# Optimization experiments

Hardware: AMD Instinct MI355X
Metric: run time of the kernel (lower is better)

The kernel has to match this reference:

```python
import jax, jax.numpy as jnp
import numpy as np
import math

NUM_HEADS = 16
HEAD_DIM = 64
D_MODEL = NUM_HEADS * HEAD_DIM  # 1024
B, S = 4, 2048

def setup_inputs() -> dict:
    key = jax.random.key(0)
    ks = jax.random.split(key, 8)
    sd = 1.0 / math.sqrt(D_MODEL)
    return {
        "hidden_states": jax.random.normal(ks[0], (B, S, D_MODEL), jnp.float32),
        "attention_mask": jnp.zeros((B, 1, 1, S), jnp.float32),
        "Wq": jax.random.normal(ks[1], (D_MODEL, D_MODEL), jnp.float32) * sd,
        "bq": jnp.zeros((D_MODEL,), jnp.float32),
        "Wk": jax.random.normal(ks[2], (D_MODEL, D_MODEL), jnp.float32) * sd,
        "bk": jnp.zeros((D_MODEL,), jnp.float32),
        "Wv": jax.random.normal(ks[3], (D_MODEL, D_MODEL), jnp.float32) * sd,
        "bv": jnp.zeros((D_MODEL,), jnp.float32),
    }

def _split_heads(x):
    # [B, S, D] -> [B, H, S, hd]
    b, s, _ = x.shape
    return x.reshape(b, s, NUM_HEADS, HEAD_DIM).transpose(0, 2, 1, 3)

def reference(hidden_states, attention_mask, Wq, bq, Wk, bk, Wv, bv):
    # Linear projections (torch nn.Linear: x @ W.T + b)
    q = _split_heads(hidden_states @ Wq.T + bq)
    k = _split_heads(hidden_states @ Wk.T + bk)
    v = _split_heads(hidden_states @ Wv.T + bv)
    scale = 1.0 / math.sqrt(HEAD_DIM)
    # [B, H, Sq, Sk] attention scores, fully materialized as in the original
    scores = jnp.einsum("bhqd,bhkd->bhqk", q, k) * scale + attention_mask
    # relusq replacement for softmax
    probs = jnp.square(jax.nn.relu(scores))
    ctx = jnp.einsum("bhqk,bhkd->bhqd", probs, v)  # [B, H, S, hd]
    b = ctx.shape[0]
    return ctx.transpose(0, 2, 1, 3).reshape(b, -1, D_MODEL)
```

## Files before the change

### kernel.cpp

```cpp
#include <hip/hip_runtime.h>


typedef __bf16 bf16x8 __attribute__((ext_vector_type(8)));
typedef __bf16 bf16x4 __attribute__((ext_vector_type(4)));
typedef __bf16 bf16x2 __attribute__((ext_vector_type(2)));
typedef short  s16x4  __attribute__((ext_vector_type(4)));
typedef float  f32x4  __attribute__((ext_vector_type(4)));
typedef float  f32x16 __attribute__((ext_vector_type(16)));
typedef float  floatx4 __attribute__((ext_vector_type(4)));
typedef unsigned u32x2 __attribute__((ext_vector_type(2)));
typedef unsigned u32x4 __attribute__((ext_vector_type(4)));

#define MFMA16(a, b, c) __builtin_amdgcn_mfma_f32_16x16x32_bf16(a, b, c, 0, 0, 0)
#define MFMA32(a, b, c) __builtin_amdgcn_mfma_f32_32x32x16_bf16(a, b, c, 0, 0, 0)

#define WAITCNT_VM0() __builtin_amdgcn_s_waitcnt(0x0F70)
#define WAITCNT_VM6() __builtin_amdgcn_s_waitcnt(0x0F76)
#define BARRIER() __builtin_amdgcn_s_barrier()
#define SETPRIO(p) __builtin_amdgcn_s_setprio(p)

__device__ __forceinline__ void glds16(const __bf16* g, __bf16* l) {
    __builtin_amdgcn_global_load_lds(
        (const __attribute__((address_space(1))) void*)g,
        (__attribute__((address_space(3))) void*)l, 16, 0, 0);
}

__global__ __launch_bounds__(256) void convert_kernel(
    const float* __restrict__ X, const float* __restrict__ Wq,
    const float* __restrict__ Wk, const float* __restrict__ Wv,
    __bf16* __restrict__ Xb, __bf16* __restrict__ Wqb,
    __bf16* __restrict__ Wkb, __bf16* __restrict__ Wvb)
{
    int blk = blockIdx.x;
    const float* src; __bf16* dst; size_t base;
    if (blk < 4096)      { src = X;  dst = Xb;  base = (size_t)blk * 2048; }
    else if (blk < 4608) { src = Wq; dst = Wqb; base = (size_t)(blk - 4096) * 2048; }
    else if (blk < 5120) { src = Wk; dst = Wkb; base = (size_t)(blk - 4608) * 2048; }
    else                 { src = Wv; dst = Wvb; base = (size_t)(blk - 5120) * 2048; }
    size_t off = base + (size_t)threadIdx.x * 8;
    floatx4 a = *(const floatx4*)(src + off);
    floatx4 c = *(const floatx4*)(src + off + 4);
    bf16x8 o;
    o[0] = (__bf16)a[0]; o[1] = (__bf16)a[1]; o[2] = (__bf16)a[2]; o[3] = (__bf16)a[3];
    o[4] = (__bf16)c[0]; o[5] = (__bf16)c[1]; o[6] = (__bf16)c[2]; o[7] = (__bf16)c[3];
    *(bf16x8*)(dst + off) = o;
}

__global__ __launch_bounds__(512, 2) void qkv_gemm_kernel(
    const __bf16* __restrict__ Xb,
    const __bf16* __restrict__ Wqb, const __bf16* __restrict__ Wkb,
    const __bf16* __restrict__ Wvb,
    const float* __restrict__ bq, const float* __restrict__ bk,
    const float* __restrict__ bv,
    __bf16* __restrict__ qws, __bf16* __restrict__ kws, __bf16* __restrict__ vws)
{
    __shared__ __bf16 As[3][256 * 64];
    __shared__ __bf16 Bs[3][128 * 64];

    const int tid  = threadIdx.x;
    const int lane = tid & 63;
    const int wave = tid >> 6;
    const int quad = lane >> 4;
    const int l16  = lane & 15;
    const int m0   = blockIdx.y * 256;

    const int sel = blockIdx.x >> 3;
    const bool vmode = (sel == 2);
    const __bf16* Wb = (sel == 0) ? Wqb : (sel == 1) ? Wkb : Wvb;
    const float* bias = (sel == 0) ? bq : (sel == 1) ? bk : bv;
    __bf16* outp = (sel == 0) ? qws : (sel == 1) ? kws : vws;
    const int n0 = (blockIdx.x & 7) * 128;

    const int wA = vmode ? (wave & 3) * 64 : (wave >> 2) * 64;
    const int wB = vmode ? (wave >> 2) * 64 : (wave & 3) * 64;

    const int srow = lane >> 3;
    const int schk = lane & 7;

    f32x4 acc[4][4] = {};

#define QKV_STAGE_A(bb, kt, i) { \
        int rb_ = wave * 32 + (i) * 8; int r_ = rb_ + srow; \
        int c_ = schk ^ (r_ & 7); \
        glds16(Xb + (size_t)(m0 + r_) * 1024 + (kt) * 64 + c_ * 8, \
               &As[bb][rb_ * 64]); }
#define QKV_STAGE_B(bb, kt, i) { \
        int rb_ = wave * 16 + (i) * 8; int r_ = rb_ + srow; \
        int c_ = schk ^ (r_ & 7); \
        glds16(Wb + (size_t)(n0 + r_) * 1024 + (kt) * 64 + c_ * 8, \
               &Bs[bb][rb_ * 64]); }

    #pragma unroll
    for (int i = 0; i < 4; ++i) QKV_STAGE_A(0, 0, i);
    #pragma unroll
    for (int i = 0; i < 2; ++i) QKV_STAGE_B(0, 0, i);
    #pragma unroll
    for (int i = 0; i < 4; ++i) QKV_STAGE_A(1, 1, i);
    #pragma unroll
    for (int i = 0; i < 2; ++i) QKV_STAGE_B(1, 1, i);
    WAITCNT_VM6();
    BARRIER();

    for (int s = 0; s < 16; ++s) {
        const int cb  = s % 3;
        const int pb  = (s + 2) % 3;
        const int kt2 = (s + 2) & 15;
        const __bf16* Pa_ = vmode ? &As[cb][0] : &Bs[cb][0];
        const __bf16* Pb_ = vmode ? &Bs[cb][0] : &As[cb][0];

        #pragma unroll
        for (int p = 0; p < 2; ++p) {
            bf16x8 af[4], bfr[4];
            #pragma unroll
            for (int a = 0; a < 4; ++a)
                af[a] = *(const bf16x8*)&Pa_[(wA + a * 16 + l16) * 64 +
                                             (((p * 4 + quad) ^ (l16 & 7)) * 8)];
            #pragma unroll
            for (int bb = 0; bb < 4; ++bb)
                bfr[bb] = *(const bf16x8*)&Pb_[(wB + bb * 16 + l16) * 64 +
                                               (((p * 4 + quad) ^ (l16 & 7)) * 8)];
            QKV_STAGE_A(pb, kt2, 2 * p);
            QKV_STAGE_A(pb, kt2, 2 * p + 1);
            QKV_STAGE_B(pb, kt2, p);

            if (p == 1) WAITCNT_VM6();
            BARRIER();

            SETPRIO(1);
            #pragma unroll
            for (int a = 0; a < 4; ++a)
                #pragma unroll
                for (int bb = 0; bb < 4; ++bb)
                    acc[a][bb] = MFMA16(af[a], bfr[bb], acc[a][bb]);
            SETPRIO(0);
            BARRIER();
        }
    }

#undef QKV_STAGE_A
#undef QKV_STAGE_B

    if (!vmode) {
        #pragma unroll
        for (int a = 0; a < 4; ++a) {
            int n = n0 + wA + a * 16 + quad * 4;
            floatx4 bv4 = *(const floatx4*)&bias[n];
            int h = n >> 6, d0 = n & 63;
            #pragma unroll
            for (int bb = 0; bb < 4; ++bb) {
                int m = m0 + wB + bb * 16 + l16;
                int bt = m >> 11, ss = m & 2047;
                bf16x4 o;
                #pragma unroll
                for (int r = 0; r < 4; ++r)
                    o[r] = (__bf16)(acc[a][bb][r] + bv4[r]);
                *(bf16x4*)&outp[((size_t)(bt * 16 + h) * 2048 + ss) * 64 + d0] = o;
            }
        }
    } else {
        #pragma unroll
        for (int a = 0; a < 4; ++a) {
            int m = m0 + wA + a * 16 + quad * 4;
            int bt = m >> 11, s0 = m & 2047;
            #pragma unroll
            for (int bb = 0; bb < 4; ++bb) {
                int n = n0 + wB + bb * 16 + l16;
                float bvv = bias[n];
                int h = n >> 6, d = n & 63;
                bf16x4 o;
                #pragma unroll
                for (int r = 0; r < 4; ++r)
                    o[r] = (__bf16)(acc[a][bb][r] + bvv);
                *(bf16x4*)&outp[((size_t)(bt * 16 + h) * 64 + d) * 2048 + s0] = o;
            }
        }
    }
}

__global__ __launch_bounds__(256, 2) void attn_kernel(
    const __bf16* __restrict__ Q, const __bf16* __restrict__ K,
    const __bf16* __restrict__ Vt, const float* __restrict__ mask,
    float* __restrict__ out)
{
    __shared__ __bf16 Ks[2][2][64 * 64];
    __shared__ __bf16 Vs[2][2][64 * 64];
    __shared__ float  Ms[2048];

    const int tid  = threadIdx.x;
    const int lane = tid & 63;
    const int wave = tid >> 6;
    const int l32  = lane & 31;
    const int hi   = lane >> 5;
    const int bh   = blockIdx.x;
    const int b    = bh >> 4;
    const int h    = bh & 15;
    const int q0w  = blockIdx.y * 256 + wave * 64;

    const __bf16* Qb = Q  + (size_t)bh * 2048 * 64;
    const __bf16* Kb = K  + (size_t)bh * 2048 * 64;
    const __bf16* Vb = Vt + (size_t)bh * 64 * 2048;
    const float*  mb = mask + b * 2048;

    const int rb = wave * 16;
    const int sr = rb + (lane >> 3);
    const int sc = ((lane & 7) ^ (sr & 7)) * 8;

    bf16x8 aq[2][4];
    #pragma unroll
    for (int qg = 0; qg < 2; ++qg)
        #pragma unroll
        for (int dk = 0; dk < 4; ++dk)
            aq[qg][dk] = *(const bf16x8*)(Qb +
                (size_t)(q0w + qg * 32 + l32) * 64 + dk * 16 + hi * 8);

    f32x16 co[2][2] = {};

    glds16(Kb + (size_t)sr * 64 + sc,              &Ks[0][0][rb * 64]);
    glds16(Kb + (size_t)(sr + 8) * 64 + sc,        &Ks[0][0][(rb + 8) * 64]);
    glds16(Kb + (size_t)(64 + sr) * 64 + sc,       &Ks[0][1][rb * 64]);
    glds16(Kb + (size_t)(64 + sr + 8) * 64 + sc,   &Ks[0][1][(rb + 8) * 64]);
    glds16(Vb + (size_t)sr * 2048 + sc,            &Vs[0][0][rb * 64]);
    glds16(Vb + (size_t)(sr + 8) * 2048 + sc,      &Vs[0][0][(rb + 8) * 64]);
    glds16(Vb + (size_t)sr * 2048 + 64 + sc,       &Vs[0][1][rb * 64]);
    glds16(Vb + (size_t)(sr + 8) * 2048 + 64 + sc, &Vs[0][1][(rb + 8) * 64]);
    glds16((const __bf16*)mb + (size_t)(wave * 2) * 512 + lane * 8,
           (__bf16*)Ms + (wave * 2) * 512);
    glds16((const __bf16*)mb + (size_t)(wave * 2 + 1) * 512 + lane * 8,
           (__bf16*)Ms + (wave * 2 + 1) * 512);
    WAITCNT_VM0();
    BARRIER();

    for (int t = 0; t < 16; ++t) {
        const int kn = ((t + 1) & 15) * 128;
        const int nb = (t + 1) & 1;
        const int cb = t & 1;
        glds16(Kb + (size_t)(kn + sr) * 64 + sc,            &Ks[nb][0][rb * 64]);
        glds16(Kb + (size_t)(kn + sr + 8) * 64 + sc,        &Ks[nb][0][(rb + 8) * 64]);
        glds16(Kb + (size_t)(kn + 64 + sr) * 64 + sc,       &Ks[nb][1][rb * 64]);
        glds16(Kb + (size_t)(kn + 64 + sr + 8) * 64 + sc,   &Ks[nb][1][(rb + 8) * 64]);
        glds16(Vb + (size_t)sr * 2048 + kn + sc,            &Vs[nb][0][rb * 64]);
        glds16(Vb + (size_t)(sr + 8) * 2048 + kn + sc,      &Vs[nb][0][(rb + 8) * 64]);
        glds16(Vb + (size_t)sr * 2048 + kn + 64 + sc,       &Vs[nb][1][rb * 64]);
        glds16(Vb + (size_t)(sr + 8) * 2048 + kn + 64 + sc, &Vs[nb][1][(rb + 8) * 64]);

        #pragma unroll
        for (int hf = 0; hf < 2; ++hf) {
            const __bf16* Kt = &Ks[cb][hf][0];
            const __bf16* Vtl = &Vs[cb][hf][0];
            const int k0 = t * 128 + hf * 64;

            bf16x8 akf[2][4];
            #pragma unroll
            for (int dk = 0; dk < 4; ++dk) {
                const int c0 = ((dk * 2 + hi) ^ (l32 & 7)) * 8;
                akf[0][dk] = *(const bf16x8*)&Kt[l32 * 64 + c0];
                akf[1][dk] = *(const bf16x8*)&Kt[(32 + l32) * 64 + c0];
            }
            f32x16 st[2][2] = {};
            SETPRIO(1);
            #pragma unroll
            for (int dk = 0; dk < 4; ++dk)
                #pragma unroll
                for (int qg = 0; qg < 2; ++qg) {
                    st[qg][0] = MFMA32(akf[0][dk], aq[qg][dk], st[qg][0]);
                    st[qg][1] = MFMA32(akf[1][dk], aq[qg][dk], st[qg][1]);
                }
            SETPRIO(0);

            bf16x8 paf0[2][2], paf1[2][2];
            const f32x4 zero4 = {};
            #pragma unroll
            for (int qg = 0; qg < 2; ++qg)
                #pragma unroll
                for (int kg = 0; kg < 2; ++kg) {
                    unsigned W[4][2];
                    #pragma unroll
                    for (int G = 0; G < 4; ++G) {
                        f32x4 v;
                        v[0] = st[qg][kg][G * 4 + 0];
                        v[1] = st[qg][kg][G * 4 + 1];
                        v[2] = st[qg][kg][G * 4 + 2];
                        v[3] = st[qg][kg][G * 4 + 3];
                        f32x4 mk = *(const f32x4*)&Ms[k0 + kg * 32 + G * 8 + hi * 4];
                        v = v * 0.125f + mk;
                        v = __builtin_elementwise_max(v, zero4);
                        v = v * v;
                        bf16x2 w0, w1;
                        w0[0] = (__bf16)v[0]; w0[1] = (__bf16)v[1];
                        w1[0] = (__bf16)v[2]; w1[1] = (__bf16)v[3];
                        W[G][0] = __builtin_bit_cast(unsigned, w0);
                        W[G][1] = __builtin_bit_cast(unsigned, w1);
                    }
                    u32x2 s00 = __builtin_amdgcn_permlane32_swap(W[0][0], W[1][0], false, false);
                    u32x2 s01 = __builtin_amdgcn_permlane32_swap(W[0][1], W[1][1], false, false);
                    u32x2 s10 = __builtin_amdgcn_permlane32_swap(W[2][0], W[3][0], false, false);
                    u32x2 s11 = __builtin_amdgcn_permlane32_swap(W[2][1], W[3][1], false, false);
                    u32x4 f0, f1;
                    f0[0] = s00[0]; f0[1] = s01[0]; f0[2] = s00[1]; f0[3] = s01[1];
                    f1[0] = s10[0]; f1[1] = s11[0]; f1[2] = s10[1]; f1[3] = s11[1];
                    paf0[qg][kg] = __builtin_bit_cast(bf16x8, f0);
                    paf1[qg][kg] = __builtin_bit_cast(bf16x8, f1);
                }

            SETPRIO(1);
            #pragma unroll
            for (int kg = 0; kg < 2; ++kg) {
                bf16x8 vb0[2], vb1[2];
                #pragma unroll
                for (int dt = 0; dt < 2; ++dt) {
                    const int d = dt * 32 + l32;
                    const int ch0 = (kg * 4 + hi) ^ (d & 7);
                    const int ch1 = (kg * 4 + 2 + hi) ^ (d & 7);
                    vb0[dt] = *(const bf16x8*)&Vtl[d * 64 + ch0 * 8];
                    vb1[dt] = *(const bf16x8*)&Vtl[d * 64 + ch1 * 8];
                }
                #pragma unroll
                for (int qg = 0; qg < 2; ++qg)
                    #pragma unroll
                    for (int dt = 0; dt < 2; ++dt) {
                        co[qg][dt] = MFMA32(paf0[qg][kg], vb0[dt], co[qg][dt]);
                        co[qg][dt] = MFMA32(paf1[qg][kg], vb1[dt], co[qg][dt]);
                    }
            }
            SETPRIO(0);
        }

        WAITCNT_VM0();
        BARRIER();
    }

    #pragma unroll
    for (int qg = 0; qg < 2; ++qg)
        #pragma unroll
        for (int r = 0; r < 16; ++r) {
            int q = q0w + qg * 32 + (r & 3) + 8 * (r >> 2) + 4 * hi;
            float* orow = &out[(((size_t)b * 2048 + q) * 16 + h) * 64];
            orow[l32]      = co[qg][0][r];
            orow[32 + l32] = co[qg][1][r];
        }
}

extern "C" void kernel_launch(void* const* d_in, const int* in_sizes, int n_in,
                              void* d_out, int out_size, void* d_ws, size_t ws_size,
                              hipStream_t stream) {
    const float* hidden = (const float*)d_in[0];
    const float* mask   = (const float*)d_in[1];
    const float* Wq     = (const float*)d_in[2];
    const float* bq     = (const float*)d_in[3];
    const float* Wk     = (const float*)d_in[4];
    const float* bk     = (const float*)d_in[5];
    const float* Wv     = (const float*)d_in[6];
    const float* bv     = (const float*)d_in[7];
    float* out = (float*)d_out;

    __bf16* qws = (__bf16*)d_ws;
    __bf16* kws = qws + (size_t)64 * 2048 * 64;
    __bf16* vws = kws + (size_t)64 * 2048 * 64;
    __bf16* Xb  = vws + (size_t)64 * 2048 * 64;
    __bf16* Wqb = Xb  + (size_t)8192 * 1024;
    __bf16* Wkb = Wqb + (size_t)1024 * 1024;
    __bf16* Wvb = Wkb + (size_t)1024 * 1024;

    convert_kernel<<<dim3(5632), dim3(256), 0, stream>>>(hidden, Wq, Wk, Wv,
                                                         Xb, Wqb, Wkb, Wvb);
    qkv_gemm_kernel<<<dim3(24, 32), dim3(512), 0, stream>>>(Xb, Wqb, Wkb, Wvb,
                                                            bq, bk, bv,
                                                            qws, kws, vws);
    attn_kernel<<<dim3(64, 8), dim3(256), 0, stream>>>(qws, kws, vws, mask, out);
}
```

Measured before the change: 234.3 us.

## Fuse fp32-to-bf16 conversion into QKV GEMM via register-staged loads

Removes the separate conversion kernel and has the QKV GEMM load fp32 X and W directly into registers, convert them to bf16 and write them to LDS with a two-stage register prefetch pipeline. This drops a full read/write pass over the activations and weights plus one kernel launch. In exchange it gives up async global-to-LDS loads and the three-stage buffer, and it shrinks the tile to 128x128 with 256 threads. Each block now re-reads fp32 data, which doubles global bytes per tile and adds per-block conversion work.

Result: slower. 266.9 us (+13.9%).

```diff
diff --git a/kernel.cpp b/kernel.cpp
--- a/kernel.cpp
+++ b/kernel.cpp
@@ -15,7 +15,6 @@
 #define MFMA32(a, b, c) __builtin_amdgcn_mfma_f32_32x32x16_bf16(a, b, c, 0, 0, 0)
 
 #define WAITCNT_VM0() __builtin_amdgcn_s_waitcnt(0x0F70)
-#define WAITCNT_VM6() __builtin_amdgcn_s_waitcnt(0x0F76)
 #define BARRIER() __builtin_amdgcn_s_barrier()
 #define SETPRIO(p) __builtin_amdgcn_s_setprio(p)
 
@@ -25,130 +24,130 @@
         (__attribute__((address_space(3))) void*)l, 16, 0, 0);
 }
 
-__global__ __launch_bounds__(256) void convert_kernel(
-    const float* __restrict__ X, const float* __restrict__ Wq,
-    const float* __restrict__ Wk, const float* __restrict__ Wv,
-    __bf16* __restrict__ Xb, __bf16* __restrict__ Wqb,
-    __bf16* __restrict__ Wkb, __bf16* __restrict__ Wvb)
-{
-    int blk = blockIdx.x;
-    const float* src; __bf16* dst; size_t base;
-    if (blk < 4096)      { src = X;  dst = Xb;  base = (size_t)blk * 2048; }
-    else if (blk < 4608) { src = Wq; dst = Wqb; base = (size_t)(blk - 4096) * 2048; }
-    else if (blk < 5120) { src = Wk; dst = Wkb; base = (size_t)(blk - 4608) * 2048; }
-    else                 { src = Wv; dst = Wvb; base = (size_t)(blk - 5120) * 2048; }
-    size_t off = base + (size_t)threadIdx.x * 8;
-    floatx4 a = *(const floatx4*)(src + off);
-    floatx4 c = *(const floatx4*)(src + off + 4);
-    bf16x8 o;
-    o[0] = (__bf16)a[0]; o[1] = (__bf16)a[1]; o[2] = (__bf16)a[2]; o[3] = (__bf16)a[3];
-    o[4] = (__bf16)c[0]; o[5] = (__bf16)c[1]; o[6] = (__bf16)c[2]; o[7] = (__bf16)c[3];
-    *(bf16x8*)(dst + off) = o;
-}
-
-__global__ __launch_bounds__(512, 2) void qkv_gemm_kernel(
-    const __bf16* __restrict__ Xb,
-    const __bf16* __restrict__ Wqb, const __bf16* __restrict__ Wkb,
-    const __bf16* __restrict__ Wvb,
+__global__ __launch_bounds__(256) void qkv_gemm_kernel(
+    const float* __restrict__ Xf,
+    const float* __restrict__ Wqf, const float* __restrict__ Wkf,
+    const float* __restrict__ Wvf,
     const float* __restrict__ bq, const float* __restrict__ bk,
     const float* __restrict__ bv,
     __bf16* __restrict__ qws, __bf16* __restrict__ kws, __bf16* __restrict__ vws)
 {
-    __shared__ __bf16 As[3][256 * 64];
-    __shared__ __bf16 Bs[3][128 * 64];
+    __shared__ __bf16 As[2][128 * 64];
+    __shared__ __bf16 Bs[2][128 * 64];
 
     const int tid  = threadIdx.x;
     const int lane = tid & 63;
     const int wave = tid >> 6;
+    const int wm   = (wave >> 1) * 64;
+    const int wn   = (wave & 1) * 64;
     const int quad = lane >> 4;
     const int l16  = lane & 15;
-    const int m0   = blockIdx.y * 256;
+    const int m0   = blockIdx.y * 128;
 
     const int sel = blockIdx.x >> 3;
     const bool vmode = (sel == 2);
-    const __bf16* Wb = (sel == 0) ? Wqb : (sel == 1) ? Wkb : Wvb;
+    const float* Wf = (sel == 0) ? Wqf : (sel == 1) ? Wkf : Wvf;
     const float* bias = (sel == 0) ? bq : (sel == 1) ? bk : bv;
     __bf16* outp = (sel == 0) ? qws : (sel == 1) ? kws : vws;
     const int n0 = (blockIdx.x & 7) * 128;
 
-    const int wA = vmode ? (wave & 3) * 64 : (wave >> 2) * 64;
-    const int wB = vmode ? (wave >> 2) * 64 : (wave & 3) * 64;
+    const int woffA = vmode ? wm : wn;
+    const int woffB = vmode ? wn : wm;
 
     const int srow = lane >> 3;
     const int schk = lane & 7;
 
     f32x4 acc[4][4] = {};
 
-#define QKV_STAGE_A(bb, kt, i) { \
-        int rb_ = wave * 32 + (i) * 8; int r_ = rb_ + srow; \
-        int c_ = schk ^ (r_ & 7); \
-        glds16(Xb + (size_t)(m0 + r_) * 1024 + (kt) * 64 + c_ * 8, \
-               &As[bb][rb_ * 64]); }
-#define QKV_STAGE_B(bb, kt, i) { \
-        int rb_ = wave * 16 + (i) * 8; int r_ = rb_ + srow; \
-        int c_ = schk ^ (r_ & 7); \
-        glds16(Wb + (size_t)(n0 + r_) * 1024 + (kt) * 64 + c_ * 8, \
-               &Bs[bb][rb_ * 64]); }
-
-    #pragma unroll
-    for (int i = 0; i < 4; ++i) QKV_STAGE_A(0, 0, i);
-    #pragma unroll
-    for (int i = 0; i < 2; ++i) QKV_STAGE_B(0, 0, i);
-    #pragma unroll
-    for (int i = 0; i < 4; ++i) QKV_STAGE_A(1, 1, i);
-    #pragma unroll
-    for (int i = 0; i < 2; ++i) QKV_STAGE_B(1, 1, i);
-    WAITCNT_VM6();
-    BARRIER();
+    int rbu[4], ru[4], cu[4];
+    #pragma unroll
+    for (int i = 0; i < 4; ++i) {
+        rbu[i] = wave * 32 + i * 8;
+        ru[i]  = rbu[i] + srow;
+        cu[i]  = (schk ^ (ru[i] & 7)) * 8;
+    }
+
+#define QKV_LOAD(dst, srcp, row, k) { \
+        size_t o_ = (size_t)(row) * 1024 + (size_t)(k); \
+        dst[0] = *(const floatx4*)((srcp) + o_); \
+        dst[1] = *(const floatx4*)((srcp) + o_ + 4); }
+
+#define QKV_CVTW(dstb, rb_, v) { \
+        bf16x8 o_; \
+        o_[0] = (__bf16)v[0][0]; o_[1] = (__bf16)v[0][1]; \
+        o_[2] = (__bf16)v[0][2]; o_[3] = (__bf16)v[0][3]; \
+        o_[4] = (__bf16)v[1][0]; o_[5] = (__bf16)v[1][1]; \
+        o_[6] = (__bf16)v[1][2]; o_[7] = (__bf16)v[1][3]; \
+        *(bf16x8*)&dstb[(rb_) * 64 + lane * 8] = o_; }
+
+    floatx4 ra[4][2], rw[4][2];
+
+    #pragma unroll
+    for (int i = 0; i < 4; ++i) {
+        QKV_LOAD(ra[i], Xf, m0 + ru[i], cu[i]);
+        QKV_LOAD(rw[i], Wf, n0 + ru[i], cu[i]);
+    }
+    #pragma unroll
+    for (int i = 0; i < 4; ++i) {
+        QKV_CVTW(As[0], rbu[i], ra[i]);
+        QKV_CVTW(Bs[0], rbu[i], rw[i]);
+    }
+    __syncthreads();
 
     for (int s = 0; s < 16; ++s) {
-        const int cb  = s % 3;
-        const int pb  = (s + 2) % 3;
-        const int kt2 = (s + 2) & 15;
-        const __bf16* Pa_ = vmode ? &As[cb][0] : &Bs[cb][0];
-        const __bf16* Pb_ = vmode ? &Bs[cb][0] : &As[cb][0];
-
-        #pragma unroll
-        for (int p = 0; p < 2; ++p) {
+        const int kn = ((s + 1) & 15) * 64;
+        const int nb = (s + 1) & 1;
+        const int bc = s & 1;
+
+        #pragma unroll
+        for (int i = 0; i < 4; ++i) {
+            QKV_LOAD(ra[i], Xf, m0 + ru[i], kn + cu[i]);
+            QKV_LOAD(rw[i], Wf, n0 + ru[i], kn + cu[i]);
+        }
+
+        const __bf16* Pa_ = vmode ? &As[bc][0] : &Bs[bc][0];
+        const __bf16* Pb_ = vmode ? &Bs[bc][0] : &As[bc][0];
+
+        SETPRIO(1);
+        #pragma unroll
+        for (int kk8 = 0; kk8 < 8; kk8 += 4) {
             bf16x8 af[4], bfr[4];
             #pragma unroll
             for (int a = 0; a < 4; ++a)
-                af[a] = *(const bf16x8*)&Pa_[(wA + a * 16 + l16) * 64 +
-                                             (((p * 4 + quad) ^ (l16 & 7)) * 8)];
+                af[a] = *(const bf16x8*)&Pa_[(woffA + a * 16 + l16) * 64 +
+                                             (((kk8 + quad) ^ (l16 & 7)) * 8)];
             #pragma unroll
             for (int bb = 0; bb < 4; ++bb)
-                bfr[bb] = *(const bf16x8*)&Pb_[(wB + bb * 16 + l16) * 64 +
-                                               (((p * 4 + quad) ^ (l16 & 7)) * 8)];
-            QKV_STAGE_A(pb, kt2, 2 * p);
-            QKV_STAGE_A(pb, kt2, 2 * p + 1);
-            QKV_STAGE_B(pb, kt2, p);
-
-            if (p == 1) WAITCNT_VM6();
-            BARRIER();
-
-            SETPRIO(1);
+                bfr[bb] = *(const bf16x8*)&Pb_[(woffB + bb * 16 + l16) * 64 +
+                                               (((kk8 + quad) ^ (l16 & 7)) * 8)];
             #pragma unroll
             for (int a = 0; a < 4; ++a)
                 #pragma unroll
                 for (int bb = 0; bb < 4; ++bb)
                     acc[a][bb] = MFMA16(af[a], bfr[bb], acc[a][bb]);
-            SETPRIO(0);
-            BARRIER();
-        }
-    }
-
-#undef QKV_STAGE_A
-#undef QKV_STAGE_B
+        }
+        SETPRIO(0);
+
+        #pragma unroll
+        for (int i = 0; i < 4; ++i) {
+            QKV_CVTW(As[nb], rbu[i], ra[i]);
+            QKV_CVTW(Bs[nb], rbu[i], rw[i]);
+        }
+        __syncthreads();
+    }
+
+#undef QKV_LOAD
+#undef QKV_CVTW
 
     if (!vmode) {
         #pragma unroll
         for (int a = 0; a < 4; ++a) {
-            int n = n0 + wA + a * 16 + quad * 4;
+            int n = n0 + woffA + a * 16 + quad * 4;
             floatx4 bv4 = *(const floatx4*)&bias[n];
             int h = n >> 6, d0 = n & 63;
             #pragma unroll
             for (int bb = 0; bb < 4; ++bb) {
-                int m = m0 + wB + bb * 16 + l16;
+                int m = m0 + woffB + bb * 16 + l16;
                 int bt = m >> 11, ss = m & 2047;
                 bf16x4 o;
                 #pragma unroll
@@ -160,11 +159,11 @@
     } else {
         #pragma unroll
         for (int a = 0; a < 4; ++a) {
-            int m = m0 + wA + a * 16 + quad * 4;
+            int m = m0 + woffA + a * 16 + quad * 4;
             int bt = m >> 11, s0 = m & 2047;
             #pragma unroll
             for (int bb = 0; bb < 4; ++bb) {
-                int n = n0 + wB + bb * 16 + l16;
+                int n = n0 + woffB + bb * 16 + l16;
                 float bvv = bias[n];
                 int h = n >> 6, d = n & 63;
                 bf16x4 o;
@@ -356,14 +355,8 @@
     __bf16* qws = (__bf16*)d_ws;
     __bf16* kws = qws + (size_t)64 * 2048 * 64;
     __bf16* vws = kws + (size_t)64 * 2048 * 64;
-    __bf16* Xb  = vws + (size_t)64 * 2048 * 64;
-    __bf16* Wqb = Xb  + (size_t)8192 * 1024;
-    __bf16* Wkb = Wqb + (size_t)1024 * 1024;
-    __bf16* Wvb = Wkb + (size_t)1024 * 1024;
-
-    convert_kernel<<<dim3(5632), dim3(256), 0, stream>>>(hidden, Wq, Wk, Wv,
-                                                         Xb, Wqb, Wkb, Wvb);
-    qkv_gemm_kernel<<<dim3(24, 32), dim3(512), 0, stream>>>(Xb, Wqb, Wkb, Wvb,
+
+    qkv_gemm_kernel<<<dim3(24, 64), dim3(256), 0, stream>>>(hidden, Wq, Wk, Wv,
                                                             bq, bk, bv,
                                                             qws, kws, vws);
     attn_kernel<<<dim3(64, 8), dim3(256), 0, stream>>>(qws, kws, vws, mask, out);
```
